# Kernel optimization log

Hardware: AMD Instinct MI355X
Metric: run time of the kernel (lower is better)

The kernel has to match this reference:

```python
import jax, jax.numpy as jnp
import numpy as np

N, C, H, W = 16, 64, 256, 256


def setup_inputs() -> dict:
    key = jax.random.key(0)
    ks = jax.random.split(key, 7)
    s = 1.0 / np.sqrt(C)
    return {
        "h": jax.random.normal(ks[0], (N, C, H, W), dtype=jnp.float32),
        "wq": jax.random.normal(ks[1], (C, C), dtype=jnp.float32) * s,
        "bq": jax.random.normal(ks[2], (C,), dtype=jnp.float32) * 0.01,
        "wk": jax.random.normal(ks[3], (C, C), dtype=jnp.float32) * s,
        "bk": jax.random.normal(ks[4], (C,), dtype=jnp.float32) * 0.01,
        "wv": jax.random.normal(ks[5], (C, C), dtype=jnp.float32) * s,
        "bv": jax.random.normal(ks[6], (C,), dtype=jnp.float32) * 0.01,
    }


def _proj(h, w, b):
    # 1x1 conv == per-pixel channel linear: (N,C,H,W) x (Cout,Cin)
    return jnp.einsum("nchw,oc->nohw", h, w) + b[None, :, None, None]


def reference(h, wq, bq, wk, bk, wv, bv):
    q = _proj(h, wq, bq)
    k = _proj(h, wk, bk)
    v = _proj(h, wv, bv)

    # NOTE: original code uses n = k.shape[-1] of the UNPERMUTED k => n = W
    scale = 1.0 / jnp.sqrt(jnp.asarray(W, dtype=q.dtype))

    # Channel-wise ROW attention: permute (N,C,H,W)->(N,W,H,C), attend over H
    attn_r = jnp.einsum("nchw,ngw->nwhg", q, jnp.einsum("ncgw->ngw" if False else "ncgw->ncgw", k)[0] if False else jnp.einsum("ncgw->ncgw", k).sum(axis=0) * 0) if False else None
    # row: q_r (n,w,h,c) @ k_r^T (n,w,c,g) -> (n,w,h,g)
    scores_r = jnp.einsum("nchw,ncgw->nwhg", q, k) * scale
    p_r = jax.nn.softmax(scores_r, axis=-1)
    out_r = jnp.einsum("nwhg,ncgw->nchw", p_r, v)  # back to (N,C,H,W)

    # Channel-wise COLUMN attention: permute (N,C,H,W)->(N,H,W,C), attend over W
    scores_c = jnp.einsum("nchw,nchu->nhwu", q, k) * scale
    p_c = jax.nn.softmax(scores_c, axis=-1)
    out_c = jnp.einsum("nhwu,nchu->nchw", p_c, v)

    attention = out_r + out_c
    return attention + h
```

## Files before the change

kernel.cpp:

```cpp
#include <hip/hip_runtime.h>


typedef unsigned short u16t;
typedef __bf16 bf16x8 __attribute__((ext_vector_type(8)));
typedef __bf16 bf16x2 __attribute__((ext_vector_type(2)));
typedef float  f32x4  __attribute__((ext_vector_type(4)));
typedef u16t   us8    __attribute__((ext_vector_type(8)));
typedef u16t   us4    __attribute__((ext_vector_type(4)));
typedef unsigned uu4  __attribute__((ext_vector_type(4)));

#define DEVINL __device__ __forceinline__

#define SCL16 0.09016844f

DEVINL u16t f2bf(float f){
    return __builtin_bit_cast(u16t, (__bf16)f);
}
DEVINL float bf2f(u16t h){
    unsigned u = ((unsigned)h) << 16;
    return __builtin_bit_cast(float, u);
}
DEVINL unsigned pk2(float lo, float hi){
    bf16x2 t; t[0] = (__bf16)lo; t[1] = (__bf16)hi;
    return __builtin_bit_cast(unsigned, t);
}
DEVINL f32x4 mfma16(bf16x8 a, bf16x8 b, f32x4 c){
    return __builtin_amdgcn_mfma_f32_16x16x32_bf16(a, b, c, 0, 0, 0);
}
DEVINL int xswz(int row, int chunk){
    return row*128 + ((chunk << 4) ^ (((row & 7) ^ ((row >> 2) & 7)) << 4));
}

__global__ __launch_bounds__(256) void transpose_kernel(const float* __restrict__ h,
                                                        u16t* __restrict__ hT){
    __shared__ float tile[64][257];
    const int bid = blockIdx.x;
    const int n = bid >> 8, y = bid & 255;
    const int tid = threadIdx.x;
    {
        const int c = tid >> 2, w0 = (tid & 3) * 64;
        const int base = ((n * 64 + c) * 256 + y) * 256 + w0;
        #pragma unroll
        for (int i = 0; i < 16; ++i){
            f32x4 v = *(const f32x4*)(h + base + i * 4);
            tile[c][w0 + i*4 + 0] = v[0];
            tile[c][w0 + i*4 + 1] = v[1];
            tile[c][w0 + i*4 + 2] = v[2];
            tile[c][w0 + i*4 + 3] = v[3];
        }
    }
    __syncthreads();
    #pragma unroll
    for (int j = 0; j < 4; ++j){
        const int task = tid + 256 * j;
        const int w = task >> 2, c0 = (task & 3) * 16;
        us8 o0, o1;
        #pragma unroll
        for (int e = 0; e < 8; ++e) o0[e] = f2bf(tile[c0 + e][w]);
        #pragma unroll
        for (int e = 0; e < 8; ++e) o1[e] = f2bf(tile[c0 + 8 + e][w]);
        const int ob = ((n * 256 + y) * 256 + w) * 64 + c0;
        *(us8*)(hT + ob)     = o0;
        *(us8*)(hT + ob + 8) = o1;
    }
}

template<int COL>
__global__ __launch_bounds__(512, 4) void attn_kernel(
    const u16t* __restrict__ Xg,
    const float* __restrict__ wq, const float* __restrict__ bq,
    const float* __restrict__ wk, const float* __restrict__ wvw,
    const float* __restrict__ bvp,
    u16t* __restrict__ Og,
    float* __restrict__ outp)
{
    __shared__ __align__(16) u16t Xs[16384];
    __shared__ __align__(16) u16t VtF[16384];
    __shared__ __align__(16) u16t AtF[4096];
    __shared__ __align__(16) float w16s[256];
    __shared__ float wkbqs[64];
    __shared__ float bvs[64];

    const int tid  = threadIdx.x;
    const int lane = tid & 63;
    const int wv   = tid >> 6;
    const int bid  = blockIdx.x;
    const int half = (bid >> 3) & 1;
    const int slice= (bid & 7) | ((bid >> 4) << 3);
    const int n    = slice >> 8;
    const int idx  = slice & 255;
    const int l15  = lane & 15;
    const int l4   = lane >> 4;
    const int nbase = n * 4194304;
    const int sbase = nbase + idx * 16384;
    const int mt   = half*8 + wv;
    const int aa   = l15 >> 2, bb = l15 & 3;
    const int hb   = l15 >> 3;
    const char* Xc = (const char*)Xs;

    {
        const int r0 = tid >> 3, cc = tid & 7;
        const int swzS = (((r0 & 7) ^ ((tid >> 5) & 7)) << 4);
        char* pdst = (char*)Xs + r0*128 + ((cc << 4) ^ swzS);
        const u16t* psrc = Xg + (COL ? (sbase + r0*64 + cc*8)
                                     : (nbase + r0*16384 + idx*64 + cc*8));
        const int gstep = COL ? 4096 : 1048576;
        #pragma unroll
        for (int pass = 0; pass < 4; ++pass){
            us8 v = *(const us8*)(psrc + pass*gstep);
            *(us8*)(pdst + pass*8192) = v;
        }
    }

    {
        const int mtA = wv >> 1;
        us8 aku[2];
        #pragma unroll
        for (int kt = 0; kt < 2; ++kt)
            #pragma unroll
            for (int e = 0; e < 8; ++e)
                aku[kt][e] = f2bf(wk[(kt*32 + l4*8 + e)*64 + mtA*16 + l15]);
        #pragma unroll
        for (int t2 = 0; t2 < 2; ++t2){
            const int ntA = (2*wv + t2) & 3;
            us8 bqu[2];
            #pragma unroll
            for (int kt = 0; kt < 2; ++kt)
                #pragma unroll
                for (int e = 0; e < 8; ++e)
                    bqu[kt][e] = f2bf(wq[(kt*32 + l4*8 + e)*64 + ntA*16 + l15]);
            f32x4 acc = {0.f,0.f,0.f,0.f};
            acc = mfma16(__builtin_bit_cast(bf16x8, aku[0]), __builtin_bit_cast(bf16x8, bqu[0]), acc);
            acc = mfma16(__builtin_bit_cast(bf16x8, aku[1]), __builtin_bit_cast(bf16x8, bqu[1]), acc);
            #pragma unroll
            for (int r = 0; r < 4; ++r){
                const int cp = mtA*16 + 4*l4 + r;
                const int cc = ntA*16 + l15;
                const int vtq  = 2*(cp>>5) + ((cp>>2)&1);
                const int mrow = 4*((cp>>3)&3) + (cp&3);
                const int f    = vtq*2 + (cc>>5);
                AtF[(f*64 + ((cc>>3)&3)*16 + mrow)*8 + (cc&7)] = f2bf(acc[r] * SCL16);
            }
        }
    }
    if (tid < 64){
        float acc = 0.f;
        for (int o = 0; o < 64; ++o) acc += wk[o*64 + tid] * bq[o];
        wkbqs[tid] = acc;
        bvs[tid] = bvp[tid];
    }
    __syncthreads();

    {
        const int ct = wv >> 1;
        bf16x8 awv[2];
        #pragma unroll
        for (int ktc = 0; ktc < 2; ++ktc){
            const float* wp = wvw + (ct*16 + l15)*64 + ktc*32 + l4*8;
            f32x4 v0 = *(const f32x4*)wp;
            f32x4 v1 = *(const f32x4*)(wp + 4);
            us8 u;
            #pragma unroll
            for (int e = 0; e < 4; ++e){ u[e] = f2bf(v0[e]); u[4+e] = f2bf(v1[e]); }
            awv[ktc] = __builtin_bit_cast(bf16x8, u);
        }
        const char* pb0 = Xc + (wv&1)*16384 + l15*128;
        const int swzE = (((l15&7) ^ aa) << 4);
        const int swzO = (((l15&7) ^ (4+aa)) << 4);
        const int cE0 = (l4<<4) ^ swzE, cE1 = ((4+l4)<<4) ^ swzE;
        const int cO0 = (l4<<4) ^ swzO, cO1 = ((4+l4)<<4) ^ swzO;
        char* pvw = (char*)VtF + (ct*8 + (wv&1)*4)*1024 + hb*256 + l4*64 + (l15&7)*2;
        #pragma unroll
        for (int t = 0; t < 8; ++t){
            const int o0 = (t&1) ? cO0 : cE0, o1 = (t&1) ? cO1 : cE1;
            bf16x8 bx0 = *(const bf16x8*)(pb0 + t*2048 + o0);
            bf16x8 bx1 = *(const bf16x8*)(pb0 + t*2048 + o1);
            f32x4 z = {0.f,0.f,0.f,0.f};
            z = mfma16(awv[0], bx0, z);
            z = mfma16(awv[1], bx1, z);
            char* pw8 = pvw + (t>>1)*1024 + (t&1)*512;
            #pragma unroll
            for (int rr = 0; rr < 4; ++rr)
                *(u16t*)(pw8 + rr*16) = f2bf(z[rr]);
        }
    }
    if (tid < 256){
        float acc = 0.f;
        #pragma unroll
        for (int cc = 0; cc < 8; ++cc){
            us8 xv = *(const us8*)(Xc + xswz(tid, cc));
            #pragma unroll
            for (int e = 0; e < 8; ++e) acc += bf2f(xv[e]) * wkbqs[cc*8 + e];
        }
        w16s[tid] = acc * SCL16;
    }
    __syncthreads();

    const int rowoff = 8*aa + bb;

    const char* pat = (const char*)AtF + lane*16;
    bf16x8 xq0 = *(const bf16x8*)(Xc + xswz(mt*16 + l15, l4));
    bf16x8 xq1 = *(const bf16x8*)(Xc + xswz(mt*16 + l15, 4 + l4));
    uu4 qp0, qp1;
    #pragma unroll
    for (int vtq = 0; vtq < 4; ++vtq){
        bf16x8 a0 = *(const bf16x8*)(pat + (vtq*2 + 0)*1024);
        bf16x8 a1 = *(const bf16x8*)(pat + (vtq*2 + 1)*1024);
        f32x4 z = {0.f,0.f,0.f,0.f};
        z = mfma16(a0, xq0, z);
        z = mfma16(a1, xq1, z);
        if (vtq < 2){
            qp0[vtq*2 + 0] = pk2(z[0], z[1]);
            qp0[vtq*2 + 1] = pk2(z[2], z[3]);
        } else {
            qp1[(vtq-2)*2 + 0] = pk2(z[0], z[1]);
            qp1[(vtq-2)*2 + 1] = pk2(z[2], z[3]);
        }
    }
    const bf16x8 qb0 = __builtin_bit_cast(bf16x8, qp0);
    const bf16x8 qb1 = __builtin_bit_cast(bf16x8, qp1);

    const int swz0 = (bb ^ (2*aa)) << 4;
    const int swz1 = ((4 + bb) ^ ((2*aa + 1) & 7)) << 4;
    const char* pv00 = Xc + rowoff*128 + ((l4<<4) ^ swz0);
    const char* pv01 = Xc + rowoff*128 + (((4+l4)<<4) ^ swz0);
    const char* pv10 = Xc + rowoff*128 + 512 + ((l4<<4) ^ swz1);
    const char* pv11 = Xc + rowoff*128 + 512 + (((4+l4)<<4) ^ swz1);
    const char* pvv = (const char*)VtF + lane*16;
    const char* pw  = (const char*)w16s + l4*32;

    uu4 onep; onep[0] = 0x3F803F80u; onep[1] = 0x3F803F80u; onep[2] = 0x3F803F80u; onep[3] = 0x3F803F80u;
    const bf16x8 onesb = __builtin_bit_cast(bf16x8, onep);

    f32x4 po[4] = {{0.f,0.f,0.f,0.f},{0.f,0.f,0.f,0.f},{0.f,0.f,0.f,0.f},{0.f,0.f,0.f,0.f}};
    f32x4 po_sum = {0.f,0.f,0.f,0.f};
    #pragma unroll
    for (int kt = 0; kt < 8; ++kt){
        uu4 tt;
        {
            bf16x8 xa0 = *(const bf16x8*)(pv00 + kt*4096);
            bf16x8 xa1 = *(const bf16x8*)(pv01 + kt*4096);
            f32x4 z = *(const f32x4*)(pw + kt*128);
            z = mfma16(xa0, qb0, z);
            z = mfma16(xa1, qb1, z);
            tt[0] = pk2(__builtin_amdgcn_exp2f(z[0]), __builtin_amdgcn_exp2f(z[1]));
            tt[1] = pk2(__builtin_amdgcn_exp2f(z[2]), __builtin_amdgcn_exp2f(z[3]));
        }
        {
            bf16x8 xa0 = *(const bf16x8*)(pv10 + kt*4096);
            bf16x8 xa1 = *(const bf16x8*)(pv11 + kt*4096);
            f32x4 z = *(const f32x4*)(pw + kt*128 + 16);
            z = mfma16(xa0, qb0, z);
            z = mfma16(xa1, qb1, z);
            tt[2] = pk2(__builtin_amdgcn_exp2f(z[0]), __builtin_amdgcn_exp2f(z[1]));
            tt[3] = pk2(__builtin_amdgcn_exp2f(z[2]), __builtin_amdgcn_exp2f(z[3]));
        }
        const bf16x8 pa = __builtin_bit_cast(bf16x8, tt);
        po_sum = mfma16(pa, onesb, po_sum);
        #pragma unroll
        for (int nt = 0; nt < 4; ++nt){
            const bf16x8 vb = *(const bf16x8*)(pvv + (nt*8 + kt)*1024);
            po[nt] = mfma16(pa, vb, po[nt]);
        }
    }
    float rs[4];
    #pragma unroll
    for (int r = 0; r < 4; ++r) rs[r] = __builtin_amdgcn_rcpf(po_sum[r]);

    u16t* OutS = VtF;

    if (!COL){
        unsigned ovp[4][2];
        #pragma unroll
        for (int nt = 0; nt < 4; ++nt){
            const int c = nt*16 + l15;
            const float b = bvs[c];
            float vr[4];
            #pragma unroll
            for (int r = 0; r < 4; ++r){
                const int y = mt*16 + 4*l4 + r;
                const float xres = bf2f(*(const u16t*)(Xc + xswz(y, c>>3) + (c&7)*2));
                vr[r] = po[nt][r]*rs[r] + b + xres;
            }
            ovp[nt][0] = pk2(vr[0], vr[1]);
            ovp[nt][1] = pk2(vr[2], vr[3]);
        }
        __syncthreads();
        #pragma unroll
        for (int nt = 0; nt < 4; ++nt){
            const int c = nt*16 + l15;
            #pragma unroll
            for (int r01 = 0; r01 < 2; ++r01){
                const int y0 = wv*16 + 4*l4 + 2*r01;
                const unsigned v = ovp[nt][r01];
                *(u16t*)((char*)OutS + y0*128 + (((c>>3)<<4) ^ ((y0&7)<<4)) + (c&7)*2) = (u16t)v;
                *(u16t*)((char*)OutS + (y0+1)*128 + (((c>>3)<<4) ^ (((y0+1)&7)<<4)) + (c&7)*2) = (u16t)(v >> 16);
            }
        }
        __syncthreads();
        #pragma unroll
        for (int p = 0; p < 2; ++p){
            const int id = p*512 + tid;
            const int yl = id >> 3, ch = id & 7;
            us8 v = *(const us8*)((const char*)OutS + yl*128 + ((ch<<4) ^ ((yl&7)<<4)));
            *(us8*)(Og + sbase + (half*128 + yl)*64 + ch*8) = v;
        }
    } else {
        __syncthreads();
        #pragma unroll
        for (int p = 0; p < 2; ++p){
            const int id = p*512 + tid;
            const int wl = id >> 3, ch = id & 7;
            us8 v = *(const us8*)(Og + nbase + (half*128 + wl)*16384 + idx*64 + ch*8);
            *(us8*)(Xs + id*8) = v;
        }
        __syncthreads();
        unsigned ovp[4][2];
        #pragma unroll
        for (int nt = 0; nt < 4; ++nt){
            const int c = nt*16 + l15;
            const float b = bvs[c];
            float vr[4];
            #pragma unroll
            for (int r = 0; r < 4; ++r){
                const int wl = wv*16 + 4*l4 + r;
                vr[r] = po[nt][r]*rs[r] + b + bf2f(Xs[wl*64 + c]);
            }
            ovp[nt][0] = pk2(vr[0], vr[1]);
            ovp[nt][1] = pk2(vr[2], vr[3]);
        }
        #pragma unroll
        for (int nt = 0; nt < 4; ++nt){
            const int c = nt*16 + l15;
            #pragma unroll
            for (int r01 = 0; r01 < 2; ++r01){
                const int w0 = wv*16 + 4*l4 + 2*r01;
                *(unsigned*)((char*)OutS + c*256 + ((w0*2) ^ ((c&7)<<4))) = ovp[nt][r01];
            }
        }
        __syncthreads();
        const int c = tid >> 3, q = tid & 7;
        const int gb = ((n*64 + c)*256 + idx)*256 + half*128;
        #pragma unroll
        for (int k = 0; k < 4; ++k){
            const int w0 = q*4 + k*32;
            us4 ov = *(const us4*)((const char*)OutS + c*256 + ((w0*2) ^ ((c&7)<<4)));
            f32x4 res;
            #pragma unroll
            for (int e = 0; e < 4; ++e) res[e] = bf2f(ov[e]);
            *(f32x4*)(outp + gb + w0) = res;
        }
    }
}

extern "C" void kernel_launch(void* const* d_in, const int* in_sizes, int n_in,
                              void* d_out, int out_size, void* d_ws, size_t ws_size,
                              hipStream_t stream){
    const float* h   = (const float*)d_in[0];
    const float* wq  = (const float*)d_in[1];
    const float* bq  = (const float*)d_in[2];
    const float* wk  = (const float*)d_in[3];
    const float* wvw = (const float*)d_in[5];
    const float* bv  = (const float*)d_in[6];
    float* out = (float*)d_out;

    u16t* hT = (u16t*)d_ws;
    u16t* Op = hT + 67108864;

    transpose_kernel<<<4096, 256, 0, stream>>>(h, hT);
    attn_kernel<0><<<8192, 512, 0, stream>>>(hT, wq, bq, wk, wvw, bv, Op, nullptr);
    attn_kernel<1><<<8192, 512, 0, stream>>>(hT, wq, bq, wk, wvw, bv, Op, out);
}
```

Measured before the change: 448.8 us.

## Load X tile via global_load_lds and swizzle V tile for packed stores

The X tile staging now goes through direct global-to-LDS loads instead of a round trip through registers, with the swizzle folded into the source column address. The V projection swaps its MFMA operands so each lane gets contiguous outputs. Those are stored as one packed 8-byte write into an XOR-swizzled VtF layout instead of four scalar 2-byte stores, and the read side applies the matching swizzle. This aims to cut register traffic and LDS bank conflicts, at the cost of relying on exact swizzle consistency and global_load_lds synchronization semantics.

```diff
diff --git a/kernel.cpp b/kernel.cpp
--- a/kernel.cpp
+++ b/kernel.cpp
@@ -8,6 +8,7 @@
 typedef u16t   us8    __attribute__((ext_vector_type(8)));
 typedef u16t   us4    __attribute__((ext_vector_type(4)));
 typedef unsigned uu4  __attribute__((ext_vector_type(4)));
+typedef unsigned uu2  __attribute__((ext_vector_type(2)));
 
 #define DEVINL __device__ __forceinline__
 
@@ -95,20 +96,23 @@
     const int sbase = nbase + idx * 16384;
     const int mt   = half*8 + wv;
     const int aa   = l15 >> 2, bb = l15 & 3;
-    const int hb   = l15 >> 3;
     const char* Xc = (const char*)Xs;
 
     {
-        const int r0 = tid >> 3, cc = tid & 7;
-        const int swzS = (((r0 & 7) ^ ((tid >> 5) & 7)) << 4);
-        char* pdst = (char*)Xs + r0*128 + ((cc << 4) ^ swzS);
-        const u16t* psrc = Xg + (COL ? (sbase + r0*64 + cc*8)
-                                     : (nbase + r0*16384 + idx*64 + cc*8));
+        const int rsub = lane >> 3;
+        const int swzl = rsub ^ ((2*wv + (lane >> 5)) & 7);
+        const int cr   = (lane & 7) ^ swzl;
+        const int row0 = wv*8 + rsub;
+        const u16t* psrc = Xg + (COL ? (sbase + row0*64 + cr*8)
+                                     : (nbase + row0*16384 + idx*64 + cr*8));
         const int gstep = COL ? 4096 : 1048576;
+        char* ldst = (char*)Xs + wv*1024;
         #pragma unroll
         for (int pass = 0; pass < 4; ++pass){
-            us8 v = *(const us8*)(psrc + pass*gstep);
-            *(us8*)(pdst + pass*8192) = v;
+            __builtin_amdgcn_global_load_lds(
+                (const __attribute__((address_space(1))) void*)(psrc + pass*gstep),
+                (__attribute__((address_space(3))) void*)(ldst + pass*8192),
+                16, 0, 0);
         }
     }
 
@@ -153,7 +157,7 @@
 
     {
         const int ct = wv >> 1;
-        bf16x8 awv[2];
+        bf16x8 bwv[2];
         #pragma unroll
         for (int ktc = 0; ktc < 2; ++ktc){
             const float* wp = wvw + (ct*16 + l15)*64 + ktc*32 + l4*8;
@@ -162,26 +166,28 @@
             us8 u;
             #pragma unroll
             for (int e = 0; e < 4; ++e){ u[e] = f2bf(v0[e]); u[4+e] = f2bf(v1[e]); }
-            awv[ktc] = __builtin_bit_cast(bf16x8, u);
+            bwv[ktc] = __builtin_bit_cast(bf16x8, u);
         }
         const char* pb0 = Xc + (wv&1)*16384 + l15*128;
         const int swzE = (((l15&7) ^ aa) << 4);
         const int swzO = (((l15&7) ^ (4+aa)) << 4);
         const int cE0 = (l4<<4) ^ swzE, cE1 = ((4+l4)<<4) ^ swzE;
         const int cO0 = (l4<<4) ^ swzO, cO1 = ((4+l4)<<4) ^ swzO;
-        char* pvw = (char*)VtF + (ct*8 + (wv&1)*4)*1024 + hb*256 + l4*64 + (l15&7)*2;
+        const int xorc = ((2*(l4>>1) + (l15>>3)) & 3) << 5;
+        char* pvw = (char*)VtF + (ct*8 + (wv&1)*4)*1024
+                  + ((256*(l4>>1) + 16*l15) ^ xorc) + 8*(l4&1);
         #pragma unroll
         for (int t = 0; t < 8; ++t){
             const int o0 = (t&1) ? cO0 : cE0, o1 = (t&1) ? cO1 : cE1;
             bf16x8 bx0 = *(const bf16x8*)(pb0 + t*2048 + o0);
             bf16x8 bx1 = *(const bf16x8*)(pb0 + t*2048 + o1);
             f32x4 z = {0.f,0.f,0.f,0.f};
-            z = mfma16(awv[0], bx0, z);
-            z = mfma16(awv[1], bx1, z);
-            char* pw8 = pvw + (t>>1)*1024 + (t&1)*512;
-            #pragma unroll
-            for (int rr = 0; rr < 4; ++rr)
-                *(u16t*)(pw8 + rr*16) = f2bf(z[rr]);
+            z = mfma16(bx0, bwv[0], z);
+            z = mfma16(bx1, bwv[1], z);
+            uu2 vz;
+            vz[0] = pk2(z[0], z[1]);
+            vz[1] = pk2(z[2], z[3]);
+            *(uu2*)(pvw + (t>>1)*1024 + (t&1)*512) = vz;
         }
     }
     if (tid < 256){
@@ -226,7 +232,7 @@
     const char* pv01 = Xc + rowoff*128 + (((4+l4)<<4) ^ swz0);
     const char* pv10 = Xc + rowoff*128 + 512 + ((l4<<4) ^ swz1);
     const char* pv11 = Xc + rowoff*128 + 512 + (((4+l4)<<4) ^ swz1);
-    const char* pvv = (const char*)VtF + lane*16;
+    const char* pvv = (const char*)VtF + ((lane*16) ^ (((lane>>3)&3) << 5));
     const char* pw  = (const char*)w16s + l4*32;
 
     uu4 onep; onep[0] = 0x3F803F80u; onep[1] = 0x3F803F80u; onep[2] = 0x3F803F80u; onep[3] = 0x3F803F80u;
```

Result: slower. 478.5 us (+6.6%).

## Process full 256-row slice per block with two query tiles per wave

Applied to the files above, without the earlier changes.

Each block now handles the whole 256-row slice instead of splitting it into two halves across two blocks. Each wave computes two 16-row query tiles, sharing the K/X fragment loads and V fragment loads across both tiles. This halves the grid and removes the duplicated slice load, V projection and key-bias precompute that each half-block used to repeat. In exchange each wave holds twice as many accumulators, which raises register pressure and may lower occupancy. The CUDA-style COL staging buffer stride grows to 512 bytes to fit 256 columns.

```diff
diff --git a/kernel.cpp b/kernel.cpp
--- a/kernel.cpp
+++ b/kernel.cpp
@@ -85,17 +85,13 @@
     const int lane = tid & 63;
     const int wv   = tid >> 6;
     const int bid  = blockIdx.x;
-    const int half = (bid >> 3) & 1;
-    const int slice= (bid & 7) | ((bid >> 4) << 3);
-    const int n    = slice >> 8;
-    const int idx  = slice & 255;
+    const int n    = bid >> 8;
+    const int idx  = bid & 255;
     const int l15  = lane & 15;
     const int l4   = lane >> 4;
     const int nbase = n * 4194304;
     const int sbase = nbase + idx * 16384;
-    const int mt   = half*8 + wv;
     const int aa   = l15 >> 2, bb = l15 & 3;
-    const int hb   = l15 >> 3;
     const char* Xc = (const char*)Xs;
 
     {
@@ -169,7 +165,7 @@
         const int swzO = (((l15&7) ^ (4+aa)) << 4);
         const int cE0 = (l4<<4) ^ swzE, cE1 = ((4+l4)<<4) ^ swzE;
         const int cO0 = (l4<<4) ^ swzO, cO1 = ((4+l4)<<4) ^ swzO;
-        char* pvw = (char*)VtF + (ct*8 + (wv&1)*4)*1024 + hb*256 + l4*64 + (l15&7)*2;
+        char* pvw = (char*)VtF + (ct*8 + (wv&1)*4)*1024 + (l15>>3)*256 + l4*64 + (l15&7)*2;
         #pragma unroll
         for (int t = 0; t < 8; ++t){
             const int o0 = (t&1) ? cO0 : cE0, o1 = (t&1) ? cO1 : cE1;
@@ -199,26 +195,32 @@
     const int rowoff = 8*aa + bb;
 
     const char* pat = (const char*)AtF + lane*16;
-    bf16x8 xq0 = *(const bf16x8*)(Xc + xswz(mt*16 + l15, l4));
-    bf16x8 xq1 = *(const bf16x8*)(Xc + xswz(mt*16 + l15, 4 + l4));
-    uu4 qp0, qp1;
+    bf16x8 xq[2][2];
+    #pragma unroll
+    for (int mi = 0; mi < 2; ++mi){
+        const int mt = wv + 8*mi;
+        xq[mi][0] = *(const bf16x8*)(Xc + xswz(mt*16 + l15, l4));
+        xq[mi][1] = *(const bf16x8*)(Xc + xswz(mt*16 + l15, 4 + l4));
+    }
+    uu4 qp[2][2];
     #pragma unroll
     for (int vtq = 0; vtq < 4; ++vtq){
         bf16x8 a0 = *(const bf16x8*)(pat + (vtq*2 + 0)*1024);
         bf16x8 a1 = *(const bf16x8*)(pat + (vtq*2 + 1)*1024);
-        f32x4 z = {0.f,0.f,0.f,0.f};
-        z = mfma16(a0, xq0, z);
-        z = mfma16(a1, xq1, z);
-        if (vtq < 2){
-            qp0[vtq*2 + 0] = pk2(z[0], z[1]);
-            qp0[vtq*2 + 1] = pk2(z[2], z[3]);
-        } else {
-            qp1[(vtq-2)*2 + 0] = pk2(z[0], z[1]);
-            qp1[(vtq-2)*2 + 1] = pk2(z[2], z[3]);
-        }
-    }
-    const bf16x8 qb0 = __builtin_bit_cast(bf16x8, qp0);
-    const bf16x8 qb1 = __builtin_bit_cast(bf16x8, qp1);
+        #pragma unroll
+        for (int mi = 0; mi < 2; ++mi){
+            f32x4 z = {0.f,0.f,0.f,0.f};
+            z = mfma16(a0, xq[mi][0], z);
+            z = mfma16(a1, xq[mi][1], z);
+            qp[mi][vtq>>1][(vtq&1)*2 + 0] = pk2(z[0], z[1]);
+            qp[mi][vtq>>1][(vtq&1)*2 + 1] = pk2(z[2], z[3]);
+        }
+    }
+    bf16x8 qb[2][2];
+    qb[0][0] = __builtin_bit_cast(bf16x8, qp[0][0]);
+    qb[0][1] = __builtin_bit_cast(bf16x8, qp[0][1]);
+    qb[1][0] = __builtin_bit_cast(bf16x8, qp[1][0]);
+    qb[1][1] = __builtin_bit_cast(bf16x8, qp[1][1]);
 
     const int swz0 = (bb ^ (2*aa)) << 4;
     const int swz1 = ((4 + bb) ^ ((2*aa + 1) & 7)) << 4;
@@ -232,119 +234,122 @@
     uu4 onep; onep[0] = 0x3F803F80u; onep[1] = 0x3F803F80u; onep[2] = 0x3F803F80u; onep[3] = 0x3F803F80u;
     const bf16x8 onesb = __builtin_bit_cast(bf16x8, onep);
 
-    f32x4 po[4] = {{0.f,0.f,0.f,0.f},{0.f,0.f,0.f,0.f},{0.f,0.f,0.f,0.f},{0.f,0.f,0.f,0.f}};
-    f32x4 po_sum = {0.f,0.f,0.f,0.f};
+    f32x4 po[2][4] = {{{0.f,0.f,0.f,0.f},{0.f,0.f,0.f,0.f},{0.f,0.f,0.f,0.f},{0.f,0.f,0.f,0.f}},
+                      {{0.f,0.f,0.f,0.f},{0.f,0.f,0.f,0.f},{0.f,0.f,0.f,0.f},{0.f,0.f,0.f,0.f}}};
+    f32x4 po_sum[2] = {{0.f,0.f,0.f,0.f},{0.f,0.f,0.f,0.f}};
+
     #pragma unroll
     for (int kt = 0; kt < 8; ++kt){
-        uu4 tt;
-        {
-            bf16x8 xa0 = *(const bf16x8*)(pv00 + kt*4096);
-            bf16x8 xa1 = *(const bf16x8*)(pv01 + kt*4096);
-            f32x4 z = *(const f32x4*)(pw + kt*128);
-            z = mfma16(xa0, qb0, z);
-            z = mfma16(xa1, qb1, z);
-            tt[0] = pk2(__builtin_amdgcn_exp2f(z[0]), __builtin_amdgcn_exp2f(z[1]));
-            tt[1] = pk2(__builtin_amdgcn_exp2f(z[2]), __builtin_amdgcn_exp2f(z[3]));
-        }
-        {
-            bf16x8 xa0 = *(const bf16x8*)(pv10 + kt*4096);
-            bf16x8 xa1 = *(const bf16x8*)(pv11 + kt*4096);
-            f32x4 z = *(const f32x4*)(pw + kt*128 + 16);
-            z = mfma16(xa0, qb0, z);
-            z = mfma16(xa1, qb1, z);
-            tt[2] = pk2(__builtin_amdgcn_exp2f(z[0]), __builtin_amdgcn_exp2f(z[1]));
-            tt[3] = pk2(__builtin_amdgcn_exp2f(z[2]), __builtin_amdgcn_exp2f(z[3]));
-        }
-        const bf16x8 pa = __builtin_bit_cast(bf16x8, tt);
-        po_sum = mfma16(pa, onesb, po_sum);
+        bf16x8 xa00 = *(const bf16x8*)(pv00 + kt*4096);
+        bf16x8 xa01 = *(const bf16x8*)(pv01 + kt*4096);
+        bf16x8 xa10 = *(const bf16x8*)(pv10 + kt*4096);
+        bf16x8 xa11 = *(const bf16x8*)(pv11 + kt*4096);
+        f32x4 cw0 = *(const f32x4*)(pw + kt*128);
+        f32x4 cw1 = *(const f32x4*)(pw + kt*128 + 16);
+        bf16x8 pa[2];
+        #pragma unroll
+        for (int mi = 0; mi < 2; ++mi){
+            uu4 tt;
+            f32x4 z0 = cw0;
+            z0 = mfma16(xa00, qb[mi][0], z0);
+            z0 = mfma16(xa01, qb[mi][1], z0);
+            tt[0] = pk2(__builtin_amdgcn_exp2f(z0[0]), __builtin_amdgcn_exp2f(z0[1]));
+            tt[1] = pk2(__builtin_amdgcn_exp2f(z0[2]), __builtin_amdgcn_exp2f(z0[3]));
+            f32x4 z1 = cw1;
+            z1 = mfma16(xa10, qb[mi][0], z1);
+            z1 = mfma16(xa11, qb[mi][1], z1);
+            tt[2] = pk2(__builtin_amdgcn_exp2f(z1[0]), __builtin_amdgcn_exp2f(z1[1]));
+            tt[3] = pk2(__builtin_amdgcn_exp2f(z1[2]), __builtin_amdgcn_exp2f(z1[3]));
+            pa[mi] = __builtin_bit_cast(bf16x8, tt);
+            po_sum[mi] = mfma16(pa[mi], onesb, po_sum[mi]);
+        }
         #pragma unroll
         for (int nt = 0; nt < 4; ++nt){
             const bf16x8 vb = *(const bf16x8*)(pvv + (nt*8 + kt)*1024);
-            po[nt] = mfma16(pa, vb, po[nt]);
-        }
-    }
-    float rs[4];
-    #pragma unroll
-    for (int r = 0; r < 4; ++r) rs[r] = __builtin_amdgcn_rcpf(po_sum[r]);
-
+            po[0][nt] = mfma16(pa[0], vb, po[0][nt]);
+            po[1][nt] = mfma16(pa[1], vb, po[1][nt]);
+        }
+    }
+
+    __syncthreads();
     u16t* OutS = VtF;
 
     if (!COL){
-        unsigned ovp[4][2];
-        #pragma unroll
-        for (int nt = 0; nt < 4; ++nt){
-            const int c = nt*16 + l15;
-            const float b = bvs[c];
-            float vr[4];
-            #pragma unroll
-            for (int r = 0; r < 4; ++r){
-                const int y = mt*16 + 4*l4 + r;
-                const float xres = bf2f(*(const u16t*)(Xc + xswz(y, c>>3) + (c&7)*2));
-                vr[r] = po[nt][r]*rs[r] + b + xres;
+        #pragma unroll
+        for (int mi = 0; mi < 2; ++mi){
+            const int mt = wv + 8*mi;
+            float rs[4];
+            #pragma unroll
+            for (int r = 0; r < 4; ++r) rs[r] = __builtin_amdgcn_rcpf(po_sum[mi][r]);
+            #pragma unroll
+            for (int nt = 0; nt < 4; ++nt){
+                const int c = nt*16 + l15;
+                const float b = bvs[c];
+                #pragma unroll
+                for (int r01 = 0; r01 < 2; ++r01){
+                    float vr[2];
+                    #pragma unroll
+                    for (int e = 0; e < 2; ++e){
+                        const int r = 2*r01 + e;
+                        const int y = mt*16 + 4*l4 + r;
+                        const float xres = bf2f(*(const u16t*)(Xc + xswz(y, c>>3) + (c&7)*2));
+                        vr[e] = po[mi][nt][r]*rs[r] + b + xres;
+                    }
+                    const int y0 = mt*16 + 4*l4 + 2*r01;
+                    const unsigned v = pk2(vr[0], vr[1]);
+                    *(u16t*)((char*)OutS + y0*128 + (((c>>3)<<4) ^ ((y0&7)<<4)) + (c&7)*2) = (u16t)v;
+                    *(u16t*)((char*)OutS + (y0+1)*128 + (((c>>3)<<4) ^ (((y0+1)&7)<<4)) + (c&7)*2) = (u16t)(v >> 16);
+                }
             }
-            ovp[nt][0] = pk2(vr[0], vr[1]);
-            ovp[nt][1] = pk2(vr[2], vr[3]);
         }
         __syncthreads();
         #pragma unroll
-        for (int nt = 0; nt < 4; ++nt){
-            const int c = nt*16 + l15;
-            #pragma unroll
-            for (int r01 = 0; r01 < 2; ++r01){
-                const int y0 = wv*16 + 4*l4 + 2*r01;
-                const unsigned v = ovp[nt][r01];
-                *(u16t*)((char*)OutS + y0*128 + (((c>>3)<<4) ^ ((y0&7)<<4)) + (c&7)*2) = (u16t)v;
-                *(u16t*)((char*)OutS + (y0+1)*128 + (((c>>3)<<4) ^ (((y0+1)&7)<<4)) + (c&7)*2) = (u16t)(v >> 16);
-            }
-        }
-        __syncthreads();
-        #pragma unroll
-        for (int p = 0; p < 2; ++p){
+        for (int p = 0; p < 4; ++p){
             const int id = p*512 + tid;
-            const int yl = id >> 3, ch = id & 7;
-            us8 v = *(const us8*)((const char*)OutS + yl*128 + ((ch<<4) ^ ((yl&7)<<4)));
-            *(us8*)(Og + sbase + (half*128 + yl)*64 + ch*8) = v;
+            const int y = id >> 3, ch = id & 7;
+            us8 v = *(const us8*)((const char*)OutS + y*128 + ((ch<<4) ^ ((y&7)<<4)));
+            *(us8*)(Og + sbase + y*64 + ch*8) = v;
         }
     } else {
-        __syncthreads();
-        #pragma unroll
-        for (int p = 0; p < 2; ++p){
+        #pragma unroll
+        for (int p = 0; p < 4; ++p){
             const int id = p*512 + tid;
             const int wl = id >> 3, ch = id & 7;
-            us8 v = *(const us8*)(Og + nbase + (half*128 + wl)*16384 + idx*64 + ch*8);
+            us8 v = *(const us8*)(Og + nbase + wl*16384 + idx*64 + ch*8);
             *(us8*)(Xs + id*8) = v;
         }
         __syncthreads();
-        unsigned ovp[4][2];
-        #pragma unroll
-        for (int nt = 0; nt < 4; ++nt){
-            const int c = nt*16 + l15;
-            const float b = bvs[c];
-            float vr[4];
-            #pragma unroll
-            for (int r = 0; r < 4; ++r){
-                const int wl = wv*16 + 4*l4 + r;
-                vr[r] = po[nt][r]*rs[r] + b + bf2f(Xs[wl*64 + c]);
-            }
-            ovp[nt][0] = pk2(vr[0], vr[1]);
-            ovp[nt][1] = pk2(vr[2], vr[3]);
-        }
-        #pragma unroll
-        for (int nt = 0; nt < 4; ++nt){
-            const int c = nt*16 + l15;
-            #pragma unroll
-            for (int r01 = 0; r01 < 2; ++r01){
-                const int w0 = wv*16 + 4*l4 + 2*r01;
-                *(unsigned*)((char*)OutS + c*256 + ((w0*2) ^ ((c&7)<<4))) = ovp[nt][r01];
+        #pragma unroll
+        for (int mi = 0; mi < 2; ++mi){
+            const int mt = wv + 8*mi;
+            float rs[4];
+            #pragma unroll
+            for (int r = 0; r < 4; ++r) rs[r] = __builtin_amdgcn_rcpf(po_sum[mi][r]);
+            #pragma unroll
+            for (int nt = 0; nt < 4; ++nt){
+                const int c = nt*16 + l15;
+                const float b = bvs[c];
+                #pragma unroll
+                for (int r01 = 0; r01 < 2; ++r01){
+                    float vr[2];
+                    #pragma unroll
+                    for (int e = 0; e < 2; ++e){
+                        const int r = 2*r01 + e;
+                        const int wl = mt*16 + 4*l4 + r;
+                        vr[e] = po[mi][nt][r]*rs[r] + b + bf2f(Xs[wl*64 + c]);
+                    }
+                    const int w0 = mt*16 + 4*l4 + 2*r01;
+                    *(unsigned*)((char*)OutS + c*512 + ((w0*2) ^ ((c&7)<<4))) = pk2(vr[0], vr[1]);
+                }
             }
         }
         __syncthreads();
         const int c = tid >> 3, q = tid & 7;
-        const int gb = ((n*64 + c)*256 + idx)*256 + half*128;
-        #pragma unroll
-        for (int k = 0; k < 4; ++k){
+        const int gb = ((n*64 + c)*256 + idx)*256;
+        #pragma unroll
+        for (int k = 0; k < 8; ++k){
             const int w0 = q*4 + k*32;
-            us4 ov = *(const us4*)((const char*)OutS + c*256 + ((w0*2) ^ ((c&7)<<4)));
+            us4 ov = *(const us4*)((const char*)OutS + c*512 + ((w0*2) ^ ((c&7)<<4)));
             f32x4 res;
             #pragma unroll
             for (int e = 0; e < 4; ++e) res[e] = bf2f(ov[e]);
@@ -368,6 +373,6 @@
     u16t* Op = hT + 67108864;
 
     transpose_kernel<<<4096, 256, 0, stream>>>(h, hT);
-    attn_kernel<0><<<8192, 512, 0, stream>>>(hT, wq, bq, wk, wvw, bv, Op, nullptr);
-    attn_kernel<1><<<8192, 512, 0, stream>>>(hT, wq, bq, wk, wvw, bv, Op, out);
-}
+    attn_kernel<0><<<4096, 512, 0, stream>>>(hT, wq, bq, wk, wvw, bv, Op, nullptr);
+    attn_kernel<1><<<4096, 512, 0, stream>>>(hT, wq, bq, wk, wvw, bv, Op, out);
+}
```

Result: faster. 379.9 us (-15.4%).
